# Kernel tuning notes

Measured on AMD Instinct MI355X. Metric: run time of the kernel, lower is better.

The kernel has to match this reference:

```python
import jax, jax.numpy as jnp
import numpy as np

N, B, T, D = 6, 4, 1024, 768
P = 3            # number of prior phases
H, Dh = 2, 32    # n_heads, head_dim
I = H * Dh       # inner_dim
EPS = 1e-5


def setup_inputs() -> dict:
    key = jax.random.key(0)
    ks = jax.random.split(key, 9)
    current_states = jax.random.normal(ks[0], (N, B, T, D), dtype=jnp.float32)
    history_states = jax.random.normal(ks[1], (P, N, B, T, D), dtype=jnp.float32)
    attention_mask = jax.random.randint(ks[2], (B, T), 0, 2, dtype=jnp.int32)
    # Linear weights stored as [in, out] (transposed nn.Linear weight)
    s = 1.0 / np.sqrt(D)
    Wq = jax.random.uniform(ks[3], (N, D, I), jnp.float32, -s, s)  # per-domain q proj
    Wk = jax.random.uniform(ks[4], (D, I), jnp.float32, -s, s)     # shared k proj
    Wv = jax.random.uniform(ks[5], (D, I), jnp.float32, -s, s)     # shared v proj
    so = 1.0 / np.sqrt(I)
    Wo = jax.random.uniform(ks[6], (N, I, D), jnp.float32, -so, so)  # per-domain out proj
    gamma = jnp.ones((N, D), jnp.float32)   # per-domain LayerNorm weight
    beta = jnp.zeros((N, D), jnp.float32)   # per-domain LayerNorm bias
    return {"current_states": current_states, "history_states": history_states,
            "attention_mask": attention_mask, "Wq": Wq, "Wk": Wk, "Wv": Wv,
            "Wo": Wo, "gamma": gamma, "beta": beta}


def reference(current_states, history_states, attention_mask, Wq, Wk, Wv, Wo, gamma, beta):
    x = current_states                                   # [N,B,T,D]
    # concat prior phases along time per domain: [N,B,P*T,D]
    prior = jnp.transpose(history_states, (1, 2, 0, 3, 4)).reshape(N, B, P * T, D)

    q = jnp.einsum('nbtd,ndi->nbti', x, Wq).reshape(N, B, T, H, Dh).transpose(0, 1, 3, 2, 4)       # [N,B,H,T,Dh]
    k = jnp.einsum('nbsd,di->nbsi', prior, Wk).reshape(N, B, P * T, H, Dh).transpose(0, 1, 3, 2, 4)  # [N,B,H,S,Dh]
    v = jnp.einsum('nbsd,di->nbsi', prior, Wv).reshape(N, B, P * T, H, Dh).transpose(0, 1, 3, 2, 4)

    scale = 1.0 / jnp.sqrt(jnp.float32(Dh))
    scores = jnp.einsum('nbhtd,nbhsd->nbhts', q, k) * scale  # [N,B,H,T,P*T]
    full_mask = jnp.tile(attention_mask.astype(jnp.float32), (1, P))  # [B,P*T]
    bias = (1.0 - full_mask)[None, :, None, None, :] * -10000.0
    attn = jax.nn.softmax(scores + bias, axis=-1)
    o = jnp.einsum('nbhts,nbhsd->nbhtd', attn, v)            # [N,B,H,T,Dh]
    o = o.transpose(0, 1, 3, 2, 4).reshape(N, B, T, I)       # [N,B,T,I]
    o = jnp.einsum('nbti,nid->nbtd', o, Wo)                  # [N,B,T,D]

    y = x + o  # residual (dropout p=0)
    mu = jnp.mean(y, axis=-1, keepdims=True)
    var = jnp.mean(jnp.square(y - mu), axis=-1, keepdims=True)
    out = (y - mu) * jax.lax.rsqrt(var + EPS)
    out = out * gamma[:, None, None, :] + beta[:, None, None, :]
    return out
```

## Files before the change

kernel.cpp:

```cpp
#include <hip/hip_runtime.h>
#include <hip/hip_bf16.h>
#include <math.h>

#define NDOM 6
#define BB 4
#define TT 1024
#define DD 768
#define PP 3
#define HH 2
#define DHH 32
#define II 64
#define SS (PP*TT)
#define NROW (NDOM*BB*TT)
#define NKVROW (NDOM*BB*SS)
#define NSPLIT 4
#define LNEPS 1e-5f

typedef unsigned int uint;
typedef uint  u32x4  __attribute__((ext_vector_type(4)));
typedef int   i32x2  __attribute__((ext_vector_type(2)));
typedef float f32x2  __attribute__((ext_vector_type(2)));
typedef float f32x4  __attribute__((ext_vector_type(4)));
typedef float f32x16 __attribute__((ext_vector_type(16)));
typedef __bf16 bf16x8 __attribute__((ext_vector_type(8)));

__device__ __forceinline__ f32x16 mfma32(u32x4 a, u32x4 b, f32x16 c) {
  return __builtin_amdgcn_mfma_f32_32x32x16_bf16(
      __builtin_bit_cast(bf16x8, a), __builtin_bit_cast(bf16x8, b), c, 0, 0, 0);
}

__device__ __forceinline__ uint pkbf(float a, float b) {
  union { __bf16 h[2]; uint u; } v;
  v.h[0] = (__bf16)a; v.h[1] = (__bf16)b;
  return v.u;
}
__device__ __forceinline__ float b2f(uint u16) {
  union { uint i; float f; } v; v.i = u16 << 16; return v.f;
}

__device__ __forceinline__ void plswap(uint a, uint b, uint& x, uint& y) {
#if __has_builtin(__builtin_amdgcn_permlane32_swap)
  i32x2 r = __builtin_amdgcn_permlane32_swap((int)a, (int)b, false, false);
  x = (uint)r.x; y = (uint)r.y;
#else
  uint sa = __shfl_xor(a, 32), sb = __shfl_xor(b, 32);
  bool h1 = (threadIdx.x & 32) != 0;
  x = h1 ? sb : a;
  y = h1 ? b : sa;
#endif
}

__global__ __launch_bounds__(256) void prep_kernel(
    const int* __restrict__ mask, const float* __restrict__ Wk,
    const float* __restrict__ Wv, const float* __restrict__ Wq,
    const float* __restrict__ Wo,
    __hip_bfloat16* __restrict__ Bkv, __hip_bfloat16* __restrict__ Bq,
    __hip_bfloat16* __restrict__ Bo, float* __restrict__ bias2)
{
  int i = blockIdx.x * 256 + threadIdx.x;
  const int N1 = 128 * 768;
  const int N2 = NDOM * 64 * 768;
  const int N3 = NDOM * 768 * 64;
  if (i < N1) {
    int c = i / 768, k = i % 768;
    float v = (c < 64) ? Wk[k * 64 + c] : Wv[k * 64 + (c - 64)];
    Bkv[i] = __float2bfloat16(v);
  } else if (i < N1 + N2) {
    int j = i - N1;
    int n = j / (64 * 768);
    int rem = j % (64 * 768);
    int c = rem / 768, k = rem % 768;
    Bq[j] = __float2bfloat16(Wq[((size_t)n * 768 + k) * 64 + c]);
  } else if (i < N1 + N2 + N3) {
    int j = i - N1 - N2;
    int n = j / (768 * 64);
    int rem = j % (768 * 64);
    int d = rem / 64, k = rem % 64;
    Bo[j] = __float2bfloat16(Wo[((size_t)n * 64 + k) * 768 + d]);
  } else if (i < N1 + N2 + N3 + BB * SS) {
    int j = i - N1 - N2 - N3;
    int b = j / SS, s = j % SS;
    bias2[j] = (1.0f - (float)mask[b * TT + (s & (TT - 1))]) * (-14426.950408889634f);
  }
}

__global__ __launch_bounds__(256) void q_gemm_kernel(
    const float* __restrict__ x, const __hip_bfloat16* __restrict__ Bq,
    __hip_bfloat16* __restrict__ Qo)
{
  __shared__ uint As[128 * 32];
  const int tid = threadIdx.x;
  const int lane = tid & 63, w = tid >> 6;
  const int wr = w >> 1, wc = w & 1;
  const int cl = lane & 31, hi = lane >> 5;
  const int brow = blockIdx.x * 128;
  const int n = brow >> 12;
  const float* Asrc = x + (size_t)brow * 768;
  const __hip_bfloat16* Bn = Bq + (size_t)n * 64 * 768;

  f32x16 acc0 = {}, acc1 = {};
  const int r0 = tid >> 3, oct = tid & 7;

  for (int kk = 0; kk < 12; ++kk) {
    __syncthreads();
#pragma unroll
    for (int g = 0; g < 4; ++g) {
      const float* ap = Asrc + (size_t)(r0 + 32 * g) * 768 + kk * 64 + oct * 8;
      float4 f0 = *(const float4*)ap;
      float4 f1 = *(const float4*)(ap + 4);
      int row = r0 + 32 * g;
      u32x4 pk = {pkbf(f0.x, f0.y), pkbf(f0.z, f0.w), pkbf(f1.x, f1.y), pkbf(f1.z, f1.w)};
      *(u32x4*)&As[row * 32 + ((oct ^ (row & 7)) << 2)] = pk;
    }
    __syncthreads();
#pragma unroll
    for (int ks = 0; ks < 4; ++ks) {
      int kg = kk * 64 + ks * 16 + hi * 8;
      u32x4 b = *(const u32x4*)(Bn + (size_t)(wc * 32 + cl) * 768 + kg);
      int ro0 = wr * 64 + cl;
      int ro1 = ro0 + 32;
      int oc = ks * 2 + hi;
      u32x4 a0 = *(const u32x4*)&As[ro0 * 32 + ((oc ^ (ro0 & 7)) << 2)];
      u32x4 a1 = *(const u32x4*)&As[ro1 * 32 + ((oc ^ (ro1 & 7)) << 2)];
      acc0 = mfma32(a0, b, acc0);
      acc1 = mfma32(a1, b, acc1);
    }
  }
  int c = wc * 32 + cl;
#pragma unroll
  for (int r = 0; r < 16; ++r) {
    int rl = (r & 3) + 8 * (r >> 2) + 4 * hi;
    Qo[(size_t)(brow + wr * 64 + rl) * 64 + c] = __float2bfloat16(acc0[r]);
    Qo[(size_t)(brow + wr * 64 + 32 + rl) * 64 + c] = __float2bfloat16(acc1[r]);
  }
}

__global__ __launch_bounds__(256) void kv_gemm_kernel(
    const float* __restrict__ hist, const __hip_bfloat16* __restrict__ Bkv,
    __hip_bfloat16* __restrict__ Kh, __hip_bfloat16* __restrict__ Vt2)
{
  __shared__ uint As[128 * 32];
  const int tid = threadIdx.x;
  const int lane = tid & 63, w = tid >> 6;
  const int wr = w >> 1, wc = w & 1;
  const int cl = lane & 31, hi = lane >> 5;
  const int brow = blockIdx.x * 128;
  const int nb = brow / SS;
  const int n = nb >> 2, b = nb & 3;
  const int s0 = brow % SS;
  const int p = s0 / TT, t0 = s0 % TT;
  const float* Asrc = hist + (((size_t)(p * NDOM + n) * BB + b) * TT + t0) * 768;

  f32x16 acc00 = {}, acc01 = {}, acc10 = {}, acc11 = {};
  const int r0 = tid >> 3, oct = tid & 7;

  for (int kk = 0; kk < 12; ++kk) {
    __syncthreads();
#pragma unroll
    for (int g = 0; g < 4; ++g) {
      const float* ap = Asrc + (size_t)(r0 + 32 * g) * 768 + kk * 64 + oct * 8;
      float4 f0 = *(const float4*)ap;
      float4 f1 = *(const float4*)(ap + 4);
      int row = r0 + 32 * g;
      u32x4 pk = {pkbf(f0.x, f0.y), pkbf(f0.z, f0.w), pkbf(f1.x, f1.y), pkbf(f1.z, f1.w)};
      *(u32x4*)&As[row * 32 + ((oct ^ (row & 7)) << 2)] = pk;
    }
    __syncthreads();
#pragma unroll
    for (int ks = 0; ks < 4; ++ks) {
      int kg = kk * 64 + ks * 16 + hi * 8;
      u32x4 b0 = *(const u32x4*)(Bkv + (size_t)(wc * 64 + cl) * 768 + kg);
      u32x4 b1 = *(const u32x4*)(Bkv + (size_t)(wc * 64 + 32 + cl) * 768 + kg);
      int ro0 = wr * 64 + cl;
      int ro1 = ro0 + 32;
      int oc = ks * 2 + hi;
      u32x4 a0 = *(const u32x4*)&As[ro0 * 32 + ((oc ^ (ro0 & 7)) << 2)];
      u32x4 a1 = *(const u32x4*)&As[ro1 * 32 + ((oc ^ (ro1 & 7)) << 2)];
      acc00 = mfma32(a0, b0, acc00);
      acc01 = mfma32(a0, b1, acc01);
      acc10 = mfma32(a1, b0, acc10);
      acc11 = mfma32(a1, b1, acc11);
    }
  }

  if (wc == 0) {
    const size_t base0 = ((size_t)(nb * 2 + 0) * SS);
    const size_t base1 = ((size_t)(nb * 2 + 1) * SS);
#pragma unroll
    for (int r = 0; r < 16; ++r) {
      int rl = (r & 3) + 8 * (r >> 2) + 4 * hi;
      int s  = s0 + wr * 64 + rl;
      Kh[(base0 + s) * 32 + cl]      = __float2bfloat16(acc00[r]);
      Kh[(base1 + s) * 32 + cl]      = __float2bfloat16(acc01[r]);
      Kh[(base0 + s + 32) * 32 + cl] = __float2bfloat16(acc10[r]);
      Kh[(base1 + s + 32) * 32 + cl] = __float2bfloat16(acc11[r]);
    }
  } else {
#pragma unroll
    for (int k = 0; k < 4; ++k) {
      int sb0 = (s0 + wr * 64 + 8 * k) >> 3;
      int sb1 = sb0 + 4;
      size_t a00 = (((size_t)(nb * 2 + 0) * (SS / 8) + sb0) * 32 + cl) * 8 + 4 * hi;
      size_t a01 = (((size_t)(nb * 2 + 1) * (SS / 8) + sb0) * 32 + cl) * 8 + 4 * hi;
      size_t a10 = (((size_t)(nb * 2 + 0) * (SS / 8) + sb1) * 32 + cl) * 8 + 4 * hi;
      size_t a11 = (((size_t)(nb * 2 + 1) * (SS / 8) + sb1) * 32 + cl) * 8 + 4 * hi;
      *(uint2*)(Vt2 + a00) = uint2{pkbf(acc00[4*k], acc00[4*k+1]), pkbf(acc00[4*k+2], acc00[4*k+3])};
      *(uint2*)(Vt2 + a01) = uint2{pkbf(acc01[4*k], acc01[4*k+1]), pkbf(acc01[4*k+2], acc01[4*k+3])};
      *(uint2*)(Vt2 + a10) = uint2{pkbf(acc10[4*k], acc10[4*k+1]), pkbf(acc10[4*k+2], acc10[4*k+3])};
      *(uint2*)(Vt2 + a11) = uint2{pkbf(acc11[4*k], acc11[4*k+1]), pkbf(acc11[4*k+2], acc11[4*k+3])};
    }
  }
}

struct KV { u32x4 k0, k1, k2, k3, v0, v1, v2, v3; };

__global__ __launch_bounds__(256) void attn_kernel(
    const __hip_bfloat16* __restrict__ Q, const __hip_bfloat16* __restrict__ Kh,
    const __hip_bfloat16* __restrict__ Vt2, const float* __restrict__ bias2,
    __hip_bfloat16* __restrict__ Op, float* __restrict__ Mp, float* __restrict__ Lp)
{
  const int tid = threadIdx.x;
  const int lane = tid & 63, w = tid >> 6;
  const int cl = lane & 31, hi = lane >> 5;
  const int bid = blockIdx.x;
  const int g = bid % 48;
  const int rest = bid / 48;
  const int sp = rest >> 3;
  const int tq = rest & 7;
  const int qtile = tq * 4 + w;
  const int h = g & 1, nb = g >> 1;
  const int b = nb & 3;
  const int qrow = nb * TT + qtile * 32;
  const int sbase = sp * (SS / NSPLIT);

  const __hip_bfloat16* Qp = Q + (size_t)(qrow + cl) * 64 + h * 32 + hi * 8;
  u32x4 qf0 = *(const u32x4*)Qp;
  u32x4 qf1 = *(const u32x4*)(Qp + 16);

  const __hip_bfloat16* Kp = Kh + ((size_t)(nb * 2 + h) * SS + sbase) * 32;
  const __hip_bfloat16* Vp = Vt2 + (size_t)(nb * 2 + h) * SS * 32 + (size_t)sbase * 32;
  const float* Bp = bias2 + b * SS + sbase + hi * 4;

  const float scale2 = 0.17677669529663687f * 1.4426950408889634f;
  const f32x2 sc2 = {scale2, scale2};

  f32x16 ot = {};
  float m = -1e30f, lsum = 0.f;

  auto loadKV = [&](int it) {
    KV t;
    const __hip_bfloat16* kp = Kp + (size_t)it * 64 * 32;
    t.k0 = *(const u32x4*)(kp + cl * 32 + hi * 8);
    t.k1 = *(const u32x4*)(kp + cl * 32 + 16 + hi * 8);
    t.k2 = *(const u32x4*)(kp + 1024 + cl * 32 + hi * 8);
    t.k3 = *(const u32x4*)(kp + 1024 + cl * 32 + 16 + hi * 8);
    const __hip_bfloat16* vp = Vp + (size_t)it * 64 * 32;
    t.v0 = *(const u32x4*)(vp + ((0 * 2 + hi) * 32 + cl) * 8);
    t.v1 = *(const u32x4*)(vp + ((1 * 2 + hi) * 32 + cl) * 8);
    t.v2 = *(const u32x4*)(vp + ((2 * 2 + hi) * 32 + cl) * 8);
    t.v3 = *(const u32x4*)(vp + ((3 * 2 + hi) * 32 + cl) * 8);
    return t;
  };

  auto compute = [&](const KV& t, int it) {
    f32x16 pz0 = {}, pz1 = {};
    pz0 = mfma32(t.k0, qf0, pz0);
    pz0 = mfma32(t.k1, qf1, pz0);
    pz1 = mfma32(t.k2, qf0, pz1);
    pz1 = mfma32(t.k3, qf1, pz1);
    const float* bp = Bp + it * 64;
    f32x4 b4[8];
#pragma unroll
    for (int q = 0; q < 8; ++q) b4[q] = *(const f32x4*)(bp + 8 * q);
    f32x2 p2[16];
#pragma unroll
    for (int i = 0; i < 8; ++i) {
      f32x4 bq0 = b4[i >> 1];
      f32x4 bq1 = b4[4 + (i >> 1)];
      f32x2 bv0 = (i & 1) ? f32x2{bq0.z, bq0.w} : f32x2{bq0.x, bq0.y};
      f32x2 bv1 = (i & 1) ? f32x2{bq1.z, bq1.w} : f32x2{bq1.x, bq1.y};
      p2[i]     = f32x2{pz0[2*i], pz0[2*i+1]} * sc2 + bv0;
      p2[8 + i] = f32x2{pz1[2*i], pz1[2*i+1]} * sc2 + bv1;
    }
    f32x2 mx = p2[0];
#pragma unroll
    for (int i = 1; i < 16; ++i) {
      mx.x = fmaxf(mx.x, p2[i].x);
      mx.y = fmaxf(mx.y, p2[i].y);
    }
    float tm = fmaxf(mx.x, mx.y);
    tm = fmaxf(tm, __shfl_xor(tm, 32));
    if (!__all(tm - m <= 8.f)) {
      float mn = fmaxf(m, tm);
      float f = exp2f(m - mn);
#pragma unroll
      for (int i = 0; i < 16; ++i) ot[i] *= f;
      lsum *= f;
      m = mn;
    }
    const f32x2 m2 = {m, m};
    f32x2 s2 = {0.f, 0.f};
#pragma unroll
    for (int i = 0; i < 16; ++i) {
      f32x2 d = p2[i] - m2;
      f32x2 e = {exp2f(d.x), exp2f(d.y)};
      p2[i] = e;
      s2 += e;
    }
    float ts = s2.x + s2.y;
    ts += __shfl_xor(ts, 32);
    lsum += ts;
    uint cv[16];
#pragma unroll
    for (int i = 0; i < 16; ++i) cv[i] = pkbf(p2[i].x, p2[i].y);
    u32x4 pf0, pf1, pf2, pf3;
    {
      uint x0, y0, x1, y1;
      plswap(cv[0], cv[2],  x0, y0); plswap(cv[1], cv[3],  x1, y1);
      pf0 = u32x4{x0, x1, y0, y1};
      plswap(cv[4], cv[6],  x0, y0); plswap(cv[5], cv[7],  x1, y1);
      pf1 = u32x4{x0, x1, y0, y1};
      plswap(cv[8], cv[10], x0, y0); plswap(cv[9], cv[11], x1, y1);
      pf2 = u32x4{x0, x1, y0, y1};
      plswap(cv[12], cv[14], x0, y0); plswap(cv[13], cv[15], x1, y1);
      pf3 = u32x4{x0, x1, y0, y1};
    }
    ot = mfma32(t.v0, pf0, ot);
    ot = mfma32(t.v1, pf1, ot);
    ot = mfma32(t.v2, pf2, ot);
    ot = mfma32(t.v3, pf3, ot);
  };

  KV cur = loadKV(0);
#pragma unroll 1
  for (int it = 0; it < 12; ++it) {
    KV nxt = loadKV(it + 1 < 12 ? it + 1 : 11);
    compute(cur, it);
    cur = nxt;
    __builtin_amdgcn_s_barrier();
  }

  __hip_bfloat16* op = Op + ((size_t)sp * NROW + qrow + cl) * 64 + h * 32 + 4 * hi;
#pragma unroll
  for (int k = 0; k < 4; ++k) {
    uint2 wv = {pkbf(ot[4*k], ot[4*k+1]), pkbf(ot[4*k+2], ot[4*k+3])};
    *(uint2*)(op + 8 * k) = wv;
  }
  if (lane < 32) {
    int mi = ((sp * 24 + nb) * 2 + h) * TT + qtile * 32 + cl;
    Mp[mi] = m;
    Lp[mi] = lsum;
  }
}

__global__ __launch_bounds__(256) void oproj_ln_kernel(
    const float* __restrict__ x, const __hip_bfloat16* __restrict__ Op,
    const float* __restrict__ Mp, const float* __restrict__ Lp,
    const __hip_bfloat16* __restrict__ Bo, const float* __restrict__ gamma,
    const float* __restrict__ beta, float* __restrict__ out)
{
  __shared__ float red[4][32][2];
  __shared__ float redf[32][2];
  const int tid = threadIdx.x;
  const int lane = tid & 63, w = tid >> 6;
  const int cl = lane & 31, hi = lane >> 5;
  const int row0 = blockIdx.x * 32;
  const int n = row0 >> 12;
  const int nb = row0 >> 10;
  const int trow = (row0 & 1023) + cl;
  const int MLS = 24 * 2 * TT;

  float wsp[2][NSPLIT];
#pragma unroll
  for (int h = 0; h < 2; ++h) {
    int mi = (nb * 2 + h) * TT + trow;
    float mv[NSPLIT], lv[NSPLIT];
#pragma unroll
    for (int sp = 0; sp < NSPLIT; ++sp) { mv[sp] = Mp[mi + sp * MLS]; lv[sp] = Lp[mi + sp * MLS]; }
    float ms = mv[0];
#pragma unroll
    for (int sp = 1; sp < NSPLIT; ++sp) ms = fmaxf(ms, mv[sp]);
    float den = 0.f;
#pragma unroll
    for (int sp = 0; sp < NSPLIT; ++sp) { wsp[h][sp] = exp2f(mv[sp] - ms); den = fmaf(lv[sp], wsp[h][sp], den); }
    float inv = 1.0f / den;
#pragma unroll
    for (int sp = 0; sp < NSPLIT; ++sp) wsp[h][sp] *= inv;
  }

  u32x4 af[4];
#pragma unroll
  for (int ks = 0; ks < 4; ++ks) {
    int h = ks >> 1;
    size_t off = (size_t)(row0 + cl) * 64 + ks * 16 + hi * 8;
    f32x2 s0 = {}, s1 = {}, s2 = {}, s3 = {};
#pragma unroll
    for (int sp = 0; sp < NSPLIT; ++sp) {
      u32x4 v = *(const u32x4*)(Op + (size_t)sp * NROW * 64 + off);
      float wv = wsp[h][sp];
      s0 += f32x2{b2f(v[0] & 0xffffu), b2f(v[0] >> 16)} * wv;
      s1 += f32x2{b2f(v[1] & 0xffffu), b2f(v[1] >> 16)} * wv;
      s2 += f32x2{b2f(v[2] & 0xffffu), b2f(v[2] >> 16)} * wv;
      s3 += f32x2{b2f(v[3] & 0xffffu), b2f(v[3] >> 16)} * wv;
    }
    af[ks] = u32x4{pkbf(s0.x, s0.y), pkbf(s1.x, s1.y), pkbf(s2.x, s2.y), pkbf(s3.x, s3.y)};
  }

  const __hip_bfloat16* Bp = Bo + ((size_t)n * 768 + w * 192 + cl) * 64 + hi * 8;
  f32x16 acc[6] = {};
#pragma unroll
  for (int ks = 0; ks < 4; ++ks) {
#pragma unroll
    for (int t = 0; t < 6; ++t) {
      u32x4 bb = *(const u32x4*)(Bp + (size_t)(t * 32) * 64 + ks * 16);
      acc[t] = mfma32(af[ks], bb, acc[t]);
    }
  }

  float s1[16], s2[16];
#pragma unroll
  for (int r = 0; r < 16; ++r) { s1[r] = 0.f; s2[r] = 0.f; }
#pragma unroll
  for (int t = 0; t < 6; ++t) {
#pragma unroll
    for (int r = 0; r < 16; ++r) {
      int R = (r & 3) + 8 * (r >> 2) + 4 * hi;
      int col = w * 192 + t * 32 + cl;
      float y = acc[t][r] + x[(size_t)(row0 + R) * 768 + col];
      acc[t][r] = y;
      s1[r] += y;
      s2[r] = fmaf(y, y, s2[r]);
    }
  }
#pragma unroll
  for (int r = 0; r < 16; ++r) {
#pragma unroll
    for (int off = 1; off < 32; off <<= 1) {
      s1[r] += __shfl_xor(s1[r], off);
      s2[r] += __shfl_xor(s2[r], off);
    }
  }
  if (cl == 0) {
#pragma unroll
    for (int r = 0; r < 16; ++r) {
      int R = (r & 3) + 8 * (r >> 2) + 4 * hi;
      red[w][R][0] = s1[r];
      red[w][R][1] = s2[r];
    }
  }
  __syncthreads();
  if (tid < 64) {
    int R = tid & 31, st = tid >> 5;
    redf[R][st] = red[0][R][st] + red[1][R][st] + red[2][R][st] + red[3][R][st];
  }
  __syncthreads();

  float gv[6], bv[6];
#pragma unroll
  for (int t = 0; t < 6; ++t) {
    int col = w * 192 + t * 32 + cl;
    gv[t] = gamma[n * 768 + col];
    bv[t] = beta[n * 768 + col];
  }
#pragma unroll
  for (int r = 0; r < 16; ++r) {
    int R = (r & 3) + 8 * (r >> 2) + 4 * hi;
    float mu = redf[R][0] * (1.0f / 768.0f);
    float var = redf[R][1] * (1.0f / 768.0f) - mu * mu;
    float rs = rsqrtf(var + LNEPS);
#pragma unroll
    for (int t = 0; t < 6; ++t) {
      int col = w * 192 + t * 32 + cl;
      out[(size_t)(row0 + R) * 768 + col] = (acc[t][r] - mu) * rs * gv[t] + bv[t];
    }
  }
}

extern "C" void kernel_launch(void* const* d_in, const int* in_sizes, int n_in,
                              void* d_out, int out_size, void* d_ws, size_t ws_size,
                              hipStream_t stream) {
  const float* x     = (const float*)d_in[0];
  const float* hist  = (const float*)d_in[1];
  const int*   mask  = (const int*)d_in[2];
  const float* Wq    = (const float*)d_in[3];
  const float* Wk    = (const float*)d_in[4];
  const float* Wv    = (const float*)d_in[5];
  const float* Wo    = (const float*)d_in[6];
  const float* gamma = (const float*)d_in[7];
  const float* beta  = (const float*)d_in[8];
  float* out = (float*)d_out;

  char* ws = (char*)d_ws;
  __hip_bfloat16* Qb  = (__hip_bfloat16*)ws;  ws += (size_t)NROW * II * 2;
  __hip_bfloat16* Kh  = (__hip_bfloat16*)ws;  ws += (size_t)NKVROW * II * 2;
  __hip_bfloat16* Vt2 = (__hip_bfloat16*)ws;  ws += (size_t)NKVROW * II * 2;
  __hip_bfloat16* Op  = (__hip_bfloat16*)ws;  ws += (size_t)NSPLIT * NROW * II * 2;
  float* Mp           = (float*)ws;           ws += (size_t)NSPLIT * 24 * 2 * TT * 4;
  float* Lp           = (float*)ws;           ws += (size_t)NSPLIT * 24 * 2 * TT * 4;
  __hip_bfloat16* Bkv = (__hip_bfloat16*)ws;  ws += (size_t)128 * 768 * 2;
  __hip_bfloat16* Bq  = (__hip_bfloat16*)ws;  ws += (size_t)NDOM * 64 * 768 * 2;
  __hip_bfloat16* Bo  = (__hip_bfloat16*)ws;  ws += (size_t)NDOM * 768 * 64 * 2;
  float* bias2        = (float*)ws;           ws += (size_t)BB * SS * 4;

  const int PREP_N = 128*768 + NDOM*64*768 + NDOM*768*64 + BB*SS;
  prep_kernel<<<(PREP_N + 255) / 256, 256, 0, stream>>>(mask, Wk, Wv, Wq, Wo, Bkv, Bq, Bo, bias2);
  q_gemm_kernel<<<NROW / 128, 256, 0, stream>>>(x, Bq, Qb);
  kv_gemm_kernel<<<NKVROW / 128, 256, 0, stream>>>(hist, Bkv, Kh, Vt2);
  attn_kernel<<<48 * 8 * NSPLIT, 256, 0, stream>>>(Qb, Kh, Vt2, bias2, Op, Mp, Lp);
  oproj_ln_kernel<<<NROW / 32, 256, 0, stream>>>(x, Op, Mp, Lp, Bo, gamma, beta, out);
}
```

Baseline: 234.7 us.

## Merge Q and KV projection GEMMs into one launch with double-buffered A tiles

The separate Q and KV projection kernels become one launch, with the block index choosing between the history (K/V) path and the current-state (Q) path. This removes a launch and the gap between the two kernels, and fills the tail of the KV grid with Q blocks. Each path also double-buffers the shared A tile and prefetches the next k-slice of fp32 input into registers while the MFMAs run on the current one, dropping one barrier per iteration. Shared memory per block doubles and register pressure rises, which may lower occupancy.

```diff
diff --git a/kernel.cpp b/kernel.cpp
--- a/kernel.cpp
+++ b/kernel.cpp
@@ -14,6 +14,8 @@
 #define NROW (NDOM*BB*TT)
 #define NKVROW (NDOM*BB*SS)
 #define NSPLIT 4
+#define NKVB (NKVROW/128)
+#define NQB  (NROW/128)
 #define LNEPS 1e-5f
 
 typedef unsigned int uint;
@@ -84,130 +86,142 @@
   }
 }
 
-__global__ __launch_bounds__(256) void q_gemm_kernel(
-    const float* __restrict__ x, const __hip_bfloat16* __restrict__ Bq,
-    __hip_bfloat16* __restrict__ Qo)
+__global__ __launch_bounds__(256) void qkv_gemm_kernel(
+    const float* __restrict__ x, const float* __restrict__ hist,
+    const __hip_bfloat16* __restrict__ Bkv, const __hip_bfloat16* __restrict__ Bq,
+    __hip_bfloat16* __restrict__ Qo, __hip_bfloat16* __restrict__ Kh,
+    __hip_bfloat16* __restrict__ Vt2)
 {
-  __shared__ uint As[128 * 32];
+  __shared__ uint As[2][128 * 32];
   const int tid = threadIdx.x;
   const int lane = tid & 63, w = tid >> 6;
   const int wr = w >> 1, wc = w & 1;
   const int cl = lane & 31, hi = lane >> 5;
-  const int brow = blockIdx.x * 128;
-  const int n = brow >> 12;
-  const float* Asrc = x + (size_t)brow * 768;
-  const __hip_bfloat16* Bn = Bq + (size_t)n * 64 * 768;
-
-  f32x16 acc0 = {}, acc1 = {};
   const int r0 = tid >> 3, oct = tid & 7;
 
-  for (int kk = 0; kk < 12; ++kk) {
-    __syncthreads();
-#pragma unroll
-    for (int g = 0; g < 4; ++g) {
-      const float* ap = Asrc + (size_t)(r0 + 32 * g) * 768 + kk * 64 + oct * 8;
-      float4 f0 = *(const float4*)ap;
-      float4 f1 = *(const float4*)(ap + 4);
-      int row = r0 + 32 * g;
-      u32x4 pk = {pkbf(f0.x, f0.y), pkbf(f0.z, f0.w), pkbf(f1.x, f1.y), pkbf(f1.z, f1.w)};
-      *(u32x4*)&As[row * 32 + ((oct ^ (row & 7)) << 2)] = pk;
-    }
-    __syncthreads();
-#pragma unroll
-    for (int ks = 0; ks < 4; ++ks) {
-      int kg = kk * 64 + ks * 16 + hi * 8;
-      u32x4 b = *(const u32x4*)(Bn + (size_t)(wc * 32 + cl) * 768 + kg);
-      int ro0 = wr * 64 + cl;
-      int ro1 = ro0 + 32;
-      int oc = ks * 2 + hi;
-      u32x4 a0 = *(const u32x4*)&As[ro0 * 32 + ((oc ^ (ro0 & 7)) << 2)];
-      u32x4 a1 = *(const u32x4*)&As[ro1 * 32 + ((oc ^ (ro1 & 7)) << 2)];
-      acc0 = mfma32(a0, b, acc0);
-      acc1 = mfma32(a1, b, acc1);
-    }
-  }
-  int c = wc * 32 + cl;
-#pragma unroll
-  for (int r = 0; r < 16; ++r) {
-    int rl = (r & 3) + 8 * (r >> 2) + 4 * hi;
-    Qo[(size_t)(brow + wr * 64 + rl) * 64 + c] = __float2bfloat16(acc0[r]);
-    Qo[(size_t)(brow + wr * 64 + 32 + rl) * 64 + c] = __float2bfloat16(acc1[r]);
-  }
-}
-
-__global__ __launch_bounds__(256) void kv_gemm_kernel(
-    const float* __restrict__ hist, const __hip_bfloat16* __restrict__ Bkv,
-    __hip_bfloat16* __restrict__ Kh, __hip_bfloat16* __restrict__ Vt2)
-{
-  __shared__ uint As[128 * 32];
-  const int tid = threadIdx.x;
-  const int lane = tid & 63, w = tid >> 6;
-  const int wr = w >> 1, wc = w & 1;
-  const int cl = lane & 31, hi = lane >> 5;
-  const int brow = blockIdx.x * 128;
-  const int nb = brow / SS;
-  const int n = nb >> 2, b = nb & 3;
-  const int s0 = brow % SS;
-  const int p = s0 / TT, t0 = s0 % TT;
-  const float* Asrc = hist + (((size_t)(p * NDOM + n) * BB + b) * TT + t0) * 768;
-
-  f32x16 acc00 = {}, acc01 = {}, acc10 = {}, acc11 = {};
-  const int r0 = tid >> 3, oct = tid & 7;
-
-  for (int kk = 0; kk < 12; ++kk) {
-    __syncthreads();
-#pragma unroll
-    for (int g = 0; g < 4; ++g) {
-      const float* ap = Asrc + (size_t)(r0 + 32 * g) * 768 + kk * 64 + oct * 8;
-      float4 f0 = *(const float4*)ap;
-      float4 f1 = *(const float4*)(ap + 4);
-      int row = r0 + 32 * g;
-      u32x4 pk = {pkbf(f0.x, f0.y), pkbf(f0.z, f0.w), pkbf(f1.x, f1.y), pkbf(f1.z, f1.w)};
-      *(u32x4*)&As[row * 32 + ((oct ^ (row & 7)) << 2)] = pk;
-    }
-    __syncthreads();
-#pragma unroll
-    for (int ks = 0; ks < 4; ++ks) {
-      int kg = kk * 64 + ks * 16 + hi * 8;
-      u32x4 b0 = *(const u32x4*)(Bkv + (size_t)(wc * 64 + cl) * 768 + kg);
-      u32x4 b1 = *(const u32x4*)(Bkv + (size_t)(wc * 64 + 32 + cl) * 768 + kg);
-      int ro0 = wr * 64 + cl;
-      int ro1 = ro0 + 32;
-      int oc = ks * 2 + hi;
-      u32x4 a0 = *(const u32x4*)&As[ro0 * 32 + ((oc ^ (ro0 & 7)) << 2)];
-      u32x4 a1 = *(const u32x4*)&As[ro1 * 32 + ((oc ^ (ro1 & 7)) << 2)];
-      acc00 = mfma32(a0, b0, acc00);
-      acc01 = mfma32(a0, b1, acc01);
-      acc10 = mfma32(a1, b0, acc10);
-      acc11 = mfma32(a1, b1, acc11);
-    }
-  }
-
-  if (wc == 0) {
-    const size_t base0 = ((size_t)(nb * 2 + 0) * SS);
-    const size_t base1 = ((size_t)(nb * 2 + 1) * SS);
+  if (blockIdx.x < NKVB) {
+    const int brow = blockIdx.x * 128;
+    const int nb = brow / SS;
+    const int n = nb >> 2, b = nb & 3;
+    const int s0 = brow % SS;
+    const int p = s0 / TT, t0 = s0 % TT;
+    const float* Asrc = hist + (((size_t)(p * NDOM + n) * BB + b) * TT + t0) * 768;
+
+    float4 a0[4], a1[4];
+    auto ldA = [&](int kk) {
+#pragma unroll
+      for (int g = 0; g < 4; ++g) {
+        const float* ap = Asrc + (size_t)(r0 + 32 * g) * 768 + kk * 64 + oct * 8;
+        a0[g] = *(const float4*)ap;
+        a1[g] = *(const float4*)(ap + 4);
+      }
+    };
+
+    f32x16 acc00 = {}, acc01 = {}, acc10 = {}, acc11 = {};
+    ldA(0);
+    for (int kk = 0; kk < 12; ++kk) {
+      uint* dst = As[kk & 1];
+#pragma unroll
+      for (int g = 0; g < 4; ++g) {
+        int row = r0 + 32 * g;
+        u32x4 pk = {pkbf(a0[g].x, a0[g].y), pkbf(a0[g].z, a0[g].w),
+                    pkbf(a1[g].x, a1[g].y), pkbf(a1[g].z, a1[g].w)};
+        *(u32x4*)&dst[row * 32 + ((oct ^ (row & 7)) << 2)] = pk;
+      }
+      __syncthreads();
+      if (kk + 1 < 12) ldA(kk + 1);
+#pragma unroll
+      for (int ks = 0; ks < 4; ++ks) {
+        int kg = kk * 64 + ks * 16 + hi * 8;
+        u32x4 b0 = *(const u32x4*)(Bkv + (size_t)(wc * 64 + cl) * 768 + kg);
+        u32x4 b1 = *(const u32x4*)(Bkv + (size_t)(wc * 64 + 32 + cl) * 768 + kg);
+        int ro0 = wr * 64 + cl;
+        int ro1 = ro0 + 32;
+        int oc = ks * 2 + hi;
+        u32x4 fa0 = *(const u32x4*)&dst[ro0 * 32 + ((oc ^ (ro0 & 7)) << 2)];
+        u32x4 fa1 = *(const u32x4*)&dst[ro1 * 32 + ((oc ^ (ro1 & 7)) << 2)];
+        acc00 = mfma32(fa0, b0, acc00);
+        acc01 = mfma32(fa0, b1, acc01);
+        acc10 = mfma32(fa1, b0, acc10);
+        acc11 = mfma32(fa1, b1, acc11);
+      }
+    }
+
+    if (wc == 0) {
+      const size_t base0 = ((size_t)(nb * 2 + 0) * SS);
+      const size_t base1 = ((size_t)(nb * 2 + 1) * SS);
+#pragma unroll
+      for (int r = 0; r < 16; ++r) {
+        int rl = (r & 3) + 8 * (r >> 2) + 4 * hi;
+        int s  = s0 + wr * 64 + rl;
+        Kh[(base0 + s) * 32 + cl]      = __float2bfloat16(acc00[r]);
+        Kh[(base1 + s) * 32 + cl]      = __float2bfloat16(acc01[r]);
+        Kh[(base0 + s + 32) * 32 + cl] = __float2bfloat16(acc10[r]);
+        Kh[(base1 + s + 32) * 32 + cl] = __float2bfloat16(acc11[r]);
+      }
+    } else {
+#pragma unroll
+      for (int k = 0; k < 4; ++k) {
+        int sb0 = (s0 + wr * 64 + 8 * k) >> 3;
+        int sb1 = sb0 + 4;
+        size_t a00 = (((size_t)(nb * 2 + 0) * (SS / 8) + sb0) * 32 + cl) * 8 + 4 * hi;
+        size_t a01 = (((size_t)(nb * 2 + 1) * (SS / 8) + sb0) * 32 + cl) * 8 + 4 * hi;
+        size_t a10 = (((size_t)(nb * 2 + 0) * (SS / 8) + sb1) * 32 + cl) * 8 + 4 * hi;
+        size_t a11 = (((size_t)(nb * 2 + 1) * (SS / 8) + sb1) * 32 + cl) * 8 + 4 * hi;
+        *(uint2*)(Vt2 + a00) = uint2{pkbf(acc00[4*k], acc00[4*k+1]), pkbf(acc00[4*k+2], acc00[4*k+3])};
+        *(uint2*)(Vt2 + a01) = uint2{pkbf(acc01[4*k], acc01[4*k+1]), pkbf(acc01[4*k+2], acc01[4*k+3])};
+        *(uint2*)(Vt2 + a10) = uint2{pkbf(acc10[4*k], acc10[4*k+1]), pkbf(acc10[4*k+2], acc10[4*k+3])};
+        *(uint2*)(Vt2 + a11) = uint2{pkbf(acc11[4*k], acc11[4*k+1]), pkbf(acc11[4*k+2], acc11[4*k+3])};
+      }
+    }
+  } else {
+    const int brow = (blockIdx.x - NKVB) * 128;
+    const int n = brow >> 12;
+    const float* Asrc = x + (size_t)brow * 768;
+    const __hip_bfloat16* Bn = Bq + (size_t)n * 64 * 768;
+
+    float4 a0[4], a1[4];
+    auto ldA = [&](int kk) {
+#pragma unroll
+      for (int g = 0; g < 4; ++g) {
+        const float* ap = Asrc + (size_t)(r0 + 32 * g) * 768 + kk * 64 + oct * 8;
+        a0[g] = *(const float4*)ap;
+        a1[g] = *(const float4*)(ap + 4);
+      }
+    };
+
+    f32x16 acc0 = {}, acc1 = {};
+    ldA(0);
+    for (int kk = 0; kk < 12; ++kk) {
+      uint* dst = As[kk & 1];
+#pragma unroll
+      for (int g = 0; g < 4; ++g) {
+        int row = r0 + 32 * g;
+        u32x4 pk = {pkbf(a0[g].x, a0[g].y), pkbf(a0[g].z, a0[g].w),
+                    pkbf(a1[g].x, a1[g].y), pkbf(a1[g].z, a1[g].w)};
+        *(u32x4*)&dst[row * 32 + ((oct ^ (row & 7)) << 2)] = pk;
+      }
+      __syncthreads();
+      if (kk + 1 < 12) ldA(kk + 1);
+#pragma unroll
+      for (int ks = 0; ks < 4; ++ks) {
+        int kg = kk * 64 + ks * 16 + hi * 8;
+        u32x4 b = *(const u32x4*)(Bn + (size_t)(wc * 32 + cl) * 768 + kg);
+        int ro0 = wr * 64 + cl;
+        int ro1 = ro0 + 32;
+        int oc = ks * 2 + hi;
+        u32x4 fa0 = *(const u32x4*)&dst[ro0 * 32 + ((oc ^ (ro0 & 7)) << 2)];
+        u32x4 fa1 = *(const u32x4*)&dst[ro1 * 32 + ((oc ^ (ro1 & 7)) << 2)];
+        acc0 = mfma32(fa0, b, acc0);
+        acc1 = mfma32(fa1, b, acc1);
+      }
+    }
+    int c = wc * 32 + cl;
 #pragma unroll
     for (int r = 0; r < 16; ++r) {
       int rl = (r & 3) + 8 * (r >> 2) + 4 * hi;
-      int s  = s0 + wr * 64 + rl;
-      Kh[(base0 + s) * 32 + cl]      = __float2bfloat16(acc00[r]);
-      Kh[(base1 + s) * 32 + cl]      = __float2bfloat16(acc01[r]);
-      Kh[(base0 + s + 32) * 32 + cl] = __float2bfloat16(acc10[r]);
-      Kh[(base1 + s + 32) * 32 + cl] = __float2bfloat16(acc11[r]);
-    }
-  } else {
-#pragma unroll
-    for (int k = 0; k < 4; ++k) {
-      int sb0 = (s0 + wr * 64 + 8 * k) >> 3;
-      int sb1 = sb0 + 4;
-      size_t a00 = (((size_t)(nb * 2 + 0) * (SS / 8) + sb0) * 32 + cl) * 8 + 4 * hi;
-      size_t a01 = (((size_t)(nb * 2 + 1) * (SS / 8) + sb0) * 32 + cl) * 8 + 4 * hi;
-      size_t a10 = (((size_t)(nb * 2 + 0) * (SS / 8) + sb1) * 32 + cl) * 8 + 4 * hi;
-      size_t a11 = (((size_t)(nb * 2 + 1) * (SS / 8) + sb1) * 32 + cl) * 8 + 4 * hi;
-      *(uint2*)(Vt2 + a00) = uint2{pkbf(acc00[4*k], acc00[4*k+1]), pkbf(acc00[4*k+2], acc00[4*k+3])};
-      *(uint2*)(Vt2 + a01) = uint2{pkbf(acc01[4*k], acc01[4*k+1]), pkbf(acc01[4*k+2], acc01[4*k+3])};
-      *(uint2*)(Vt2 + a10) = uint2{pkbf(acc10[4*k], acc10[4*k+1]), pkbf(acc10[4*k+2], acc10[4*k+3])};
-      *(uint2*)(Vt2 + a11) = uint2{pkbf(acc11[4*k], acc11[4*k+1]), pkbf(acc11[4*k+2], acc11[4*k+3])};
+      Qo[(size_t)(brow + wr * 64 + rl) * 64 + c] = __float2bfloat16(acc0[r]);
+      Qo[(size_t)(brow + wr * 64 + 32 + rl) * 64 + c] = __float2bfloat16(acc1[r]);
     }
   }
 }
@@ -504,8 +518,7 @@
 
   const int PREP_N = 128*768 + NDOM*64*768 + NDOM*768*64 + BB*SS;
   prep_kernel<<<(PREP_N + 255) / 256, 256, 0, stream>>>(mask, Wk, Wv, Wq, Wo, Bkv, Bq, Bo, bias2);
-  q_gemm_kernel<<<NROW / 128, 256, 0, stream>>>(x, Bq, Qb);
-  kv_gemm_kernel<<<NKVROW / 128, 256, 0, stream>>>(hist, Bkv, Kh, Vt2);
+  qkv_gemm_kernel<<<NKVB + NQB, 256, 0, stream>>>(x, hist, Bkv, Bq, Qb, Kh, Vt2);
   attn_kernel<<<48 * 8 * NSPLIT, 256, 0, stream>>>(Qb, Kh, Vt2, bias2, Op, Mp, Lp);
   oproj_ln_kernel<<<NROW / 32, 256, 0, stream>>>(x, Op, Mp, Lp, Bo, gamma, beta, out);
 }
```

Result: no change. 230.3 us (-1.9%).
